# Performance work log

Hardware: AMD Instinct MI355X
Metric: run time of the kernel (lower is better)

The kernel has to match this reference:

```python
import jax, jax.numpy as jnp
import numpy as np

B, S, H = 32, 1024, 512  # batch, src_len, hidden_dim


def setup_inputs() -> dict:
    key = jax.random.key(0)
    k1, k2, k3, k4, k5 = jax.random.split(key, 5)
    hidden = jax.random.normal(k1, (B, H), dtype=jnp.float32)
    encoder_outputs = jax.random.normal(k2, (B, S, 2 * H), dtype=jnp.float32)
    # nn.Linear(3H, H): weight stored here as [3H, H] (input-major) with bias [H]
    W = jax.random.normal(k3, (3 * H, H), dtype=jnp.float32) / np.sqrt(3 * H)
    b = jax.random.normal(k4, (H,), dtype=jnp.float32) * 0.01
    v = jax.random.normal(k5, (H,), dtype=jnp.float32) / np.sqrt(H)
    return {"hidden": hidden, "encoder_outputs": encoder_outputs, "W": W, "b": b, "v": v}


def reference(hidden, encoder_outputs, W, b, v):
    # concat((repeat(hidden), encoder_outputs)) @ W  ==  hidden @ W[:H] (broadcast) + enc @ W[H:]
    Wh, We = W[:H], W[H:]                         # [H,H], [2H,H]
    h_proj = hidden @ Wh                           # [B,H]
    e_proj = jnp.einsum('bse,eh->bsh', encoder_outputs, We)  # [B,S,H]
    energy = jnp.tanh(h_proj[:, None, :] + e_proj + b)       # [B,S,H]
    # bmm(v[B,1,H], energy^T[B,H,S]) -> scores [B,S]
    scores = jnp.einsum('bsh,h->bs', energy, v)
    return jax.nn.softmax(scores, axis=1)
```

## Files before the change

kernel.cpp:

```cpp
#include <hip/hip_runtime.h>
#include <math.h>

#define B_ 32
#define S_ 1024
#define H_ 512
#define K_ 1024
#define M_ (B_ * S_)

typedef __attribute__((ext_vector_type(8))) short bf16x8;
typedef __attribute__((ext_vector_type(4))) float f32x4;

#define AST 40

__device__ __forceinline__ void split_bf16(float f, unsigned short& hi, unsigned short& lo) {
    unsigned u = __float_as_uint(f);
    unsigned rh = (u + 0x7fffu + ((u >> 16) & 1u)) >> 16;
    hi = (unsigned short)rh;
    float fh = __uint_as_float(rh << 16);
    float r = f - fh;
    unsigned ur = __float_as_uint(r);
    unsigned rl = (ur + 0x7fffu + ((ur >> 16) & 1u)) >> 16;
    lo = (unsigned short)rl;
}

__global__ __launch_bounds__(256) void hproj_kernel(
    const float* __restrict__ hidden, const float* __restrict__ W,
    const float* __restrict__ bias, float* __restrict__ hb)
{
    const int tid = threadIdx.x;
    const int h0  = blockIdx.x * 64;
    const int b   = blockIdx.y;
    const int h   = h0 + (tid & 63);
    const int ks  = tid >> 6;
    const float* hrow = hidden + b * H_;
    float acc = 0.f;
    #pragma unroll 8
    for (int k = ks * 128; k < ks * 128 + 128; ++k)
        acc = fmaf(hrow[k], W[(size_t)k * H_ + h], acc);
    __shared__ float red[4][64];
    red[ks][tid & 63] = acc;
    __syncthreads();
    if (tid < 64)
        hb[b * H_ + h0 + tid] = red[0][tid] + red[1][tid] + red[2][tid] + red[3][tid]
                              + bias[h0 + tid];
}

__global__ __launch_bounds__(256) void conv_we_kernel(
    const float* __restrict__ We, unsigned short* __restrict__ Wh,
    unsigned short* __restrict__ Wl)
{
    __shared__ float t[32][33];
    const int tx = threadIdx.x & 31, ty = threadIdx.x >> 5;
    const int k0 = blockIdx.x * 32, n0 = blockIdx.y * 32;
    #pragma unroll
    for (int j = 0; j < 4; ++j) {
        const int k = ty + 8 * j;
        t[k][tx] = We[(size_t)(k0 + k) * H_ + n0 + tx];
    }
    __syncthreads();
    #pragma unroll
    for (int j = 0; j < 4; ++j) {
        const int n = ty + 8 * j;
        unsigned short hi, lo;
        split_bf16(t[tx][n], hi, lo);
        Wh[(size_t)(n0 + n) * K_ + k0 + tx] = hi;
        Wl[(size_t)(n0 + n) * K_ + k0 + tx] = lo;
    }
}

__global__ __launch_bounds__(256, 3) void fused_attn_gemm_mfma(
    const float* __restrict__ EO,
    const unsigned short* __restrict__ Bth,
    const unsigned short* __restrict__ Btl,
    const float* __restrict__ hb,
    const float* __restrict__ v,
    float* __restrict__ partial)
{
    __shared__ unsigned short Ah[128 * AST];
    __shared__ unsigned short Al[128 * AST];
    __shared__ unsigned short Bh[128 * AST];
    __shared__ unsigned short Bl[128 * AST];

    const int tid  = threadIdx.x;
    const int nt   = blockIdx.x;
    const int mt   = blockIdx.y;
    const int row0 = mt * 128;
    const int col0 = nt * 128;
    const int batch = row0 >> 10;

    const int lane   = tid & 63;
    const int wave   = tid >> 6;
    const int wm     = wave >> 1, wn = wave & 1;
    const int lanelo = lane & 15, quad = lane >> 4;

    f32x4 acc[4][4];
    #pragma unroll
    for (int i = 0; i < 4; ++i)
        #pragma unroll
        for (int j = 0; j < 4; ++j)
            acc[i][j] = (f32x4){0.f, 0.f, 0.f, 0.f};

    for (int k0 = 0; k0 < K_; k0 += 32) {
        #pragma unroll
        for (int q = 0; q < 4; ++q) {
            const int f = tid + 256 * q;
            const int m = f >> 3, c = f & 7;
            const float4 av = *reinterpret_cast<const float4*>(
                EO + (size_t)(row0 + m) * K_ + k0 + c * 4);
            union { unsigned short us[4]; uint2 u2; } ph, pl;
            split_bf16(av.x, ph.us[0], pl.us[0]);
            split_bf16(av.y, ph.us[1], pl.us[1]);
            split_bf16(av.z, ph.us[2], pl.us[2]);
            split_bf16(av.w, ph.us[3], pl.us[3]);
            *reinterpret_cast<uint2*>(&Ah[m * AST + c * 4]) = ph.u2;
            *reinterpret_cast<uint2*>(&Al[m * AST + c * 4]) = pl.u2;
        }
        #pragma unroll
        for (int q = 0; q < 2; ++q) {
            const int s = tid + 256 * q;
            const int n = s >> 2, qq = s & 3;
            const size_t g = (size_t)(col0 + n) * K_ + k0 + qq * 8;
            *reinterpret_cast<uint4*>(&Bh[n * AST + qq * 8]) =
                *reinterpret_cast<const uint4*>(Bth + g);
            *reinterpret_cast<uint4*>(&Bl[n * AST + qq * 8]) =
                *reinterpret_cast<const uint4*>(Btl + g);
        }
        __syncthreads();

        bf16x8 a_h[4], a_l[4], b_h[4], b_l[4];
        #pragma unroll
        for (int fi = 0; fi < 4; ++fi) {
            const int m = wm * 64 + fi * 16 + lanelo;
            a_h[fi] = *reinterpret_cast<const bf16x8*>(&Ah[m * AST + quad * 8]);
            a_l[fi] = *reinterpret_cast<const bf16x8*>(&Al[m * AST + quad * 8]);
            const int n = wn * 64 + fi * 16 + lanelo;
            b_h[fi] = *reinterpret_cast<const bf16x8*>(&Bh[n * AST + quad * 8]);
            b_l[fi] = *reinterpret_cast<const bf16x8*>(&Bl[n * AST + quad * 8]);
        }
        #pragma unroll
        for (int fi = 0; fi < 4; ++fi)
            #pragma unroll
            for (int fj = 0; fj < 4; ++fj) {
                acc[fi][fj] = __builtin_amdgcn_mfma_f32_16x16x32_bf16(
                    a_h[fi], b_h[fj], acc[fi][fj], 0, 0, 0);
                acc[fi][fj] = __builtin_amdgcn_mfma_f32_16x16x32_bf16(
                    a_h[fi], b_l[fj], acc[fi][fj], 0, 0, 0);
                acc[fi][fj] = __builtin_amdgcn_mfma_f32_16x16x32_bf16(
                    a_l[fi], b_h[fj], acc[fi][fj], 0, 0, 0);
            }
        __syncthreads();
    }

    const float* hb_row = hb + batch * H_;
    float hbv[4], vv[4];
    #pragma unroll
    for (int fj = 0; fj < 4; ++fj) {
        const int c = col0 + wn * 64 + fj * 16 + lanelo;
        hbv[fj] = hb_row[c];
        vv[fj]  = v[c];
    }
    float* red = reinterpret_cast<float*>(Ah);
    #pragma unroll
    for (int fi = 0; fi < 4; ++fi)
        #pragma unroll
        for (int r = 0; r < 4; ++r) {
            float rs = 0.f;
            #pragma unroll
            for (int fj = 0; fj < 4; ++fj)
                rs = fmaf(tanhf(acc[fi][fj][r] + hbv[fj]), vv[fj], rs);
            rs += __shfl_xor(rs, 1, 64);
            rs += __shfl_xor(rs, 2, 64);
            rs += __shfl_xor(rs, 4, 64);
            rs += __shfl_xor(rs, 8, 64);
            if (lanelo == 0) {
                const int row = wm * 64 + fi * 16 + quad * 4 + r;
                red[row * 2 + wn] = rs;
            }
        }
    __syncthreads();
    if (tid < 128)
        partial[(size_t)nt * M_ + row0 + tid] = red[tid * 2] + red[tid * 2 + 1];
}

#define BM 128
#define BN 128
#define BK 32
#define PAD 4
__global__ __launch_bounds__(256) void fused_attn_gemm_fp32(
    const float* __restrict__ EO, const float* __restrict__ We,
    const float* __restrict__ hb, const float* __restrict__ v,
    float* __restrict__ partial)
{
    __shared__ float As[BK][BM + PAD];
    __shared__ float Bs[BK][BN + PAD];
    const int tid = threadIdx.x;
    const int mt = blockIdx.x, nt = blockIdx.y;
    const int row0 = mt * BM, col0 = nt * BN;
    const int batch = row0 / S_;
    const int tx = tid & 15, ty = tid >> 4;
    float acc[8][8];
    #pragma unroll
    for (int i = 0; i < 8; ++i)
        #pragma unroll
        for (int j = 0; j < 8; ++j) acc[i][j] = 0.0f;
    for (int k0 = 0; k0 < K_; k0 += BK) {
        #pragma unroll
        for (int q = 0; q < 4; ++q) {
            const int f = tid + 256 * q;
            const int m = f >> 3, kq = f & 7;
            const float4 av = *reinterpret_cast<const float4*>(
                EO + (size_t)(row0 + m) * K_ + k0 + kq * 4);
            As[kq * 4 + 0][m] = av.x; As[kq * 4 + 1][m] = av.y;
            As[kq * 4 + 2][m] = av.z; As[kq * 4 + 3][m] = av.w;
        }
        #pragma unroll
        for (int q = 0; q < 4; ++q) {
            const int f = tid + 256 * q;
            const int k = f >> 5, cq = f & 31;
            *reinterpret_cast<float4*>(&Bs[k][cq * 4]) =
                *reinterpret_cast<const float4*>(We + (size_t)(k0 + k) * H_ + col0 + cq * 4);
        }
        __syncthreads();
        #pragma unroll
        for (int kk = 0; kk < BK; ++kk) {
            const float4 a0 = *reinterpret_cast<const float4*>(&As[kk][ty * 4]);
            const float4 a1 = *reinterpret_cast<const float4*>(&As[kk][64 + ty * 4]);
            const float4 b0 = *reinterpret_cast<const float4*>(&Bs[kk][tx * 4]);
            const float4 b1 = *reinterpret_cast<const float4*>(&Bs[kk][64 + tx * 4]);
            const float a[8] = {a0.x, a0.y, a0.z, a0.w, a1.x, a1.y, a1.z, a1.w};
            const float b[8] = {b0.x, b0.y, b0.z, b0.w, b1.x, b1.y, b1.z, b1.w};
            #pragma unroll
            for (int i = 0; i < 8; ++i)
                #pragma unroll
                for (int j = 0; j < 8; ++j)
                    acc[i][j] = fmaf(a[i], b[j], acc[i][j]);
        }
        __syncthreads();
    }
    const float* hb_row = hb + batch * H_;
    float* red = &As[0][0];
    #pragma unroll
    for (int i = 0; i < 8; ++i) {
        const int rloc = (i < 4) ? (ty * 4 + i) : (64 + ty * 4 + i - 4);
        float rs = 0.0f;
        #pragma unroll
        for (int j = 0; j < 8; ++j) {
            const int cloc = (j < 4) ? (tx * 4 + j) : (64 + tx * 4 + j - 4);
            const int c = col0 + cloc;
            rs = fmaf(tanhf(acc[i][j] + hb_row[c]), v[c], rs);
        }
        red[rloc * 17 + tx] = rs;
    }
    __syncthreads();
    if (tid < BM) {
        float s = 0.0f;
        #pragma unroll
        for (int t = 0; t < 16; ++t) s += red[tid * 17 + t];
        partial[(size_t)nt * M_ + row0 + tid] = s;
    }
}

__global__ __launch_bounds__(256) void softmax_kernel(
    const float* __restrict__ partial, float* __restrict__ out)
{
    const int b = blockIdx.x;
    const int tid = threadIdx.x;
    float val[4];
    float lmax = -3.0e38f;
    #pragma unroll
    for (int q = 0; q < 4; ++q) {
        const int idx = b * S_ + tid + 256 * q;
        float sum = partial[idx] + partial[M_ + idx] + partial[2 * M_ + idx] +
                    partial[3 * M_ + idx];
        val[q] = sum;
        lmax = fmaxf(lmax, sum);
    }
    #pragma unroll
    for (int off = 32; off > 0; off >>= 1)
        lmax = fmaxf(lmax, __shfl_down(lmax, off, 64));
    __shared__ float wmax[4];
    if ((tid & 63) == 0) wmax[tid >> 6] = lmax;
    __syncthreads();
    const float gmax = fmaxf(fmaxf(wmax[0], wmax[1]), fmaxf(wmax[2], wmax[3]));
    float lsum = 0.0f;
    #pragma unroll
    for (int q = 0; q < 4; ++q) {
        val[q] = expf(val[q] - gmax);
        lsum += val[q];
    }
    #pragma unroll
    for (int off = 32; off > 0; off >>= 1)
        lsum += __shfl_down(lsum, off, 64);
    __shared__ float wsum[4];
    if ((tid & 63) == 0) wsum[tid >> 6] = lsum;
    __syncthreads();
    const float inv = 1.0f / (wsum[0] + wsum[1] + wsum[2] + wsum[3]);
    #pragma unroll
    for (int q = 0; q < 4; ++q)
        out[b * S_ + tid + 256 * q] = val[q] * inv;
}

extern "C" void kernel_launch(void* const* d_in, const int* in_sizes, int n_in,
                              void* d_out, int out_size, void* d_ws, size_t ws_size,
                              hipStream_t stream) {
    const float* hidden = (const float*)d_in[0];
    const float* EO     = (const float*)d_in[1];
    const float* W      = (const float*)d_in[2];
    const float* bias   = (const float*)d_in[3];
    const float* v      = (const float*)d_in[4];
    float* out          = (float*)d_out;

    float* hb      = (float*)d_ws;
    float* partial = hb + B_ * H_;
    unsigned short* Wth = (unsigned short*)(partial + 4 * M_);
    unsigned short* Wtl = Wth + (size_t)H_ * K_;
    const size_t needed = (size_t)(B_ * H_ + 4 * M_) * sizeof(float)
                        + (size_t)H_ * K_ * 2 * sizeof(unsigned short);

    const float* We = W + (size_t)H_ * H_;

    hproj_kernel<<<dim3(8, B_), 256, 0, stream>>>(hidden, W, bias, hb);
    if (ws_size >= needed) {
        conv_we_kernel<<<dim3(K_ / 32, H_ / 32), 256, 0, stream>>>(We, Wth, Wtl);
        fused_attn_gemm_mfma<<<dim3(4, M_ / 128), 256, 0, stream>>>(EO, Wth, Wtl, hb, v, partial);
    } else {
        fused_attn_gemm_fp32<<<dim3(M_ / BM, 4), 256, 0, stream>>>(EO, We, hb, v, partial);
    }
    softmax_kernel<<<B_, 256, 0, stream>>>(partial, out);
}
```

Before: 327.6 us.

## Pre-split encoder outputs to bf16 hi/lo and stream tiles via async global-to-LDS loads

A separate kernel now converts the encoder outputs once into bf16 hi/lo arrays in workspace. The GEMM then loads A and B tiles straight into LDS with global_load_lds, using an XOR-swizzled layout to avoid bank conflicts. The aim is to drop the per-tile fp32-to-bf16 split (repeated across the 4 column tiles) and the register round trip from the GEMM loop. The cost is an extra pass that reads 128MB and writes 128MB, plus a much larger workspace requirement; the old in-kernel path remains as a fallback and the fp32 fallback is removed.

```diff
diff --git a/kernel.cpp b/kernel.cpp
--- a/kernel.cpp
+++ b/kernel.cpp
@@ -9,8 +9,6 @@
 
 typedef __attribute__((ext_vector_type(8))) short bf16x8;
 typedef __attribute__((ext_vector_type(4))) float f32x4;
-
-#define AST 40
 
 __device__ __forceinline__ void split_bf16(float f, unsigned short& hi, unsigned short& lo) {
     unsigned u = __float_as_uint(f);
@@ -21,6 +19,32 @@
     unsigned ur = __float_as_uint(r);
     unsigned rl = (ur + 0x7fffu + ((ur >> 16) & 1u)) >> 16;
     lo = (unsigned short)rl;
+}
+
+__device__ __forceinline__ void async_copy16(const void* g, void* l) {
+    __builtin_amdgcn_global_load_lds(
+        (const __attribute__((address_space(1))) void*)g,
+        (__attribute__((address_space(3))) void*)l, 16, 0, 0);
+}
+
+__global__ __launch_bounds__(256) void split_eo_kernel(
+    const float* __restrict__ EO, unsigned short* __restrict__ EOh,
+    unsigned short* __restrict__ EOl)
+{
+    const size_t i = ((size_t)blockIdx.x * 256 + threadIdx.x) * 8;
+    const float4 a = *reinterpret_cast<const float4*>(EO + i);
+    const float4 b = *reinterpret_cast<const float4*>(EO + i + 4);
+    union { unsigned short us[8]; uint4 u4; } h, l;
+    split_bf16(a.x, h.us[0], l.us[0]);
+    split_bf16(a.y, h.us[1], l.us[1]);
+    split_bf16(a.z, h.us[2], l.us[2]);
+    split_bf16(a.w, h.us[3], l.us[3]);
+    split_bf16(b.x, h.us[4], l.us[4]);
+    split_bf16(b.y, h.us[5], l.us[5]);
+    split_bf16(b.z, h.us[6], l.us[6]);
+    split_bf16(b.w, h.us[7], l.us[7]);
+    *reinterpret_cast<uint4*>(EOh + i) = h.u4;
+    *reinterpret_cast<uint4*>(EOl + i) = l.u4;
 }
 
 __global__ __launch_bounds__(256) void hproj_kernel(
@@ -68,18 +92,17 @@
     }
 }
 
-__global__ __launch_bounds__(256, 3) void fused_attn_gemm_mfma(
-    const float* __restrict__ EO,
-    const unsigned short* __restrict__ Bth,
-    const unsigned short* __restrict__ Btl,
-    const float* __restrict__ hb,
-    const float* __restrict__ v,
+__global__ __launch_bounds__(256, 3) void gemm_mfma_pre(
+    const unsigned short* __restrict__ EOh, const unsigned short* __restrict__ EOl,
+    const unsigned short* __restrict__ Bth, const unsigned short* __restrict__ Btl,
+    const float* __restrict__ hb, const float* __restrict__ v,
     float* __restrict__ partial)
 {
-    __shared__ unsigned short Ah[128 * AST];
-    __shared__ unsigned short Al[128 * AST];
-    __shared__ unsigned short Bh[128 * AST];
-    __shared__ unsigned short Bl[128 * AST];
+    __shared__ unsigned short lds[4 * 128 * 32];
+    unsigned short* Ah = lds;
+    unsigned short* Al = lds + 4096;
+    unsigned short* Bh = lds + 8192;
+    unsigned short* Bl = lds + 12288;
 
     const int tid  = threadIdx.x;
     const int nt   = blockIdx.x;
@@ -93,6 +116,21 @@
     const int wm     = wave >> 1, wn = wave & 1;
     const int lanelo = lane & 15, quad = lane >> 4;
 
+    const int rl = lane >> 2;
+    const int qs = lane & 3;
+
+    size_t ga[2], gb[2];
+    int ldsoff[2];
+    #pragma unroll
+    for (int j = 0; j < 2; ++j) {
+        const int iss = wave * 2 + j;
+        const int r   = iss * 16 + rl;
+        const int qg  = qs ^ ((r >> 1) & 3);
+        ga[j] = (size_t)(row0 + r) * K_ + qg * 8;
+        gb[j] = (size_t)(col0 + r) * K_ + qg * 8;
+        ldsoff[j] = iss * 512;
+    }
+
     f32x4 acc[4][4];
     #pragma unroll
     for (int i = 0; i < 4; ++i)
@@ -102,40 +140,25 @@
 
     for (int k0 = 0; k0 < K_; k0 += 32) {
         #pragma unroll
-        for (int q = 0; q < 4; ++q) {
-            const int f = tid + 256 * q;
-            const int m = f >> 3, c = f & 7;
-            const float4 av = *reinterpret_cast<const float4*>(
-                EO + (size_t)(row0 + m) * K_ + k0 + c * 4);
-            union { unsigned short us[4]; uint2 u2; } ph, pl;
-            split_bf16(av.x, ph.us[0], pl.us[0]);
-            split_bf16(av.y, ph.us[1], pl.us[1]);
-            split_bf16(av.z, ph.us[2], pl.us[2]);
-            split_bf16(av.w, ph.us[3], pl.us[3]);
-            *reinterpret_cast<uint2*>(&Ah[m * AST + c * 4]) = ph.u2;
-            *reinterpret_cast<uint2*>(&Al[m * AST + c * 4]) = pl.u2;
-        }
-        #pragma unroll
-        for (int q = 0; q < 2; ++q) {
-            const int s = tid + 256 * q;
-            const int n = s >> 2, qq = s & 3;
-            const size_t g = (size_t)(col0 + n) * K_ + k0 + qq * 8;
-            *reinterpret_cast<uint4*>(&Bh[n * AST + qq * 8]) =
-                *reinterpret_cast<const uint4*>(Bth + g);
-            *reinterpret_cast<uint4*>(&Bl[n * AST + qq * 8]) =
-                *reinterpret_cast<const uint4*>(Btl + g);
+        for (int j = 0; j < 2; ++j) {
+            async_copy16(EOh + ga[j] + k0, Ah + ldsoff[j]);
+            async_copy16(EOl + ga[j] + k0, Al + ldsoff[j]);
+            async_copy16(Bth + gb[j] + k0, Bh + ldsoff[j]);
+            async_copy16(Btl + gb[j] + k0, Bl + ldsoff[j]);
         }
         __syncthreads();
 
         bf16x8 a_h[4], a_l[4], b_h[4], b_l[4];
         #pragma unroll
         for (int fi = 0; fi < 4; ++fi) {
-            const int m = wm * 64 + fi * 16 + lanelo;
-            a_h[fi] = *reinterpret_cast<const bf16x8*>(&Ah[m * AST + quad * 8]);
-            a_l[fi] = *reinterpret_cast<const bf16x8*>(&Al[m * AST + quad * 8]);
-            const int n = wn * 64 + fi * 16 + lanelo;
-            b_h[fi] = *reinterpret_cast<const bf16x8*>(&Bh[n * AST + quad * 8]);
-            b_l[fi] = *reinterpret_cast<const bf16x8*>(&Bl[n * AST + quad * 8]);
+            const int m  = wm * 64 + fi * 16 + lanelo;
+            const int sa = quad ^ ((m >> 1) & 3);
+            a_h[fi] = *reinterpret_cast<const bf16x8*>(&Ah[m * 32 + sa * 8]);
+            a_l[fi] = *reinterpret_cast<const bf16x8*>(&Al[m * 32 + sa * 8]);
+            const int n  = wn * 64 + fi * 16 + lanelo;
+            const int sb = quad ^ ((n >> 1) & 3);
+            b_h[fi] = *reinterpret_cast<const bf16x8*>(&Bh[n * 32 + sb * 8]);
+            b_l[fi] = *reinterpret_cast<const bf16x8*>(&Bl[n * 32 + sb * 8]);
         }
         #pragma unroll
         for (int fi = 0; fi < 4; ++fi)
@@ -159,7 +182,7 @@
         hbv[fj] = hb_row[c];
         vv[fj]  = v[c];
     }
-    float* red = reinterpret_cast<float*>(Ah);
+    float* red = reinterpret_cast<float*>(lds);
     #pragma unroll
     for (int fi = 0; fi < 4; ++fi)
         #pragma unroll
@@ -182,82 +205,107 @@
         partial[(size_t)nt * M_ + row0 + tid] = red[tid * 2] + red[tid * 2 + 1];
 }
 
-#define BM 128
-#define BN 128
-#define BK 32
-#define PAD 4
-__global__ __launch_bounds__(256) void fused_attn_gemm_fp32(
-    const float* __restrict__ EO, const float* __restrict__ We,
-    const float* __restrict__ hb, const float* __restrict__ v,
-    float* __restrict__ partial)
-{
-    __shared__ float As[BK][BM + PAD];
-    __shared__ float Bs[BK][BN + PAD];
-    const int tid = threadIdx.x;
-    const int mt = blockIdx.x, nt = blockIdx.y;
-    const int row0 = mt * BM, col0 = nt * BN;
-    const int batch = row0 / S_;
-    const int tx = tid & 15, ty = tid >> 4;
-    float acc[8][8];
-    #pragma unroll
-    for (int i = 0; i < 8; ++i)
-        #pragma unroll
-        for (int j = 0; j < 8; ++j) acc[i][j] = 0.0f;
-    for (int k0 = 0; k0 < K_; k0 += BK) {
+#define AST 40
+__global__ __launch_bounds__(256, 3) void fused_attn_gemm_mfma(
+    const float* __restrict__ EO, const unsigned short* __restrict__ Bth,
+    const unsigned short* __restrict__ Btl, const float* __restrict__ hb,
+    const float* __restrict__ v, float* __restrict__ partial)
+{
+    __shared__ unsigned short Ah[128 * AST];
+    __shared__ unsigned short Al[128 * AST];
+    __shared__ unsigned short Bh[128 * AST];
+    __shared__ unsigned short Bl[128 * AST];
+    const int tid  = threadIdx.x;
+    const int nt   = blockIdx.x;
+    const int mt   = blockIdx.y;
+    const int row0 = mt * 128, col0 = nt * 128;
+    const int batch = row0 >> 10;
+    const int lane = tid & 63, wave = tid >> 6;
+    const int wm = wave >> 1, wn = wave & 1;
+    const int lanelo = lane & 15, quad = lane >> 4;
+    f32x4 acc[4][4];
+    #pragma unroll
+    for (int i = 0; i < 4; ++i)
+        #pragma unroll
+        for (int j = 0; j < 4; ++j) acc[i][j] = (f32x4){0.f, 0.f, 0.f, 0.f};
+    for (int k0 = 0; k0 < K_; k0 += 32) {
         #pragma unroll
         for (int q = 0; q < 4; ++q) {
             const int f = tid + 256 * q;
-            const int m = f >> 3, kq = f & 7;
+            const int m = f >> 3, c = f & 7;
             const float4 av = *reinterpret_cast<const float4*>(
-                EO + (size_t)(row0 + m) * K_ + k0 + kq * 4);
-            As[kq * 4 + 0][m] = av.x; As[kq * 4 + 1][m] = av.y;
-            As[kq * 4 + 2][m] = av.z; As[kq * 4 + 3][m] = av.w;
-        }
-        #pragma unroll
-        for (int q = 0; q < 4; ++q) {
-            const int f = tid + 256 * q;
-            const int k = f >> 5, cq = f & 31;
-            *reinterpret_cast<float4*>(&Bs[k][cq * 4]) =
-                *reinterpret_cast<const float4*>(We + (size_t)(k0 + k) * H_ + col0 + cq * 4);
+                EO + (size_t)(row0 + m) * K_ + k0 + c * 4);
+            union { unsigned short us[4]; uint2 u2; } ph, pl;
+            split_bf16(av.x, ph.us[0], pl.us[0]);
+            split_bf16(av.y, ph.us[1], pl.us[1]);
+            split_bf16(av.z, ph.us[2], pl.us[2]);
+            split_bf16(av.w, ph.us[3], pl.us[3]);
+            *reinterpret_cast<uint2*>(&Ah[m * AST + c * 4]) = ph.u2;
+            *reinterpret_cast<uint2*>(&Al[m * AST + c * 4]) = pl.u2;
+        }
+        #pragma unroll
+        for (int q = 0; q < 2; ++q) {
+            const int s = tid + 256 * q;
+            const int n = s >> 2, qq = s & 3;
+            const size_t g = (size_t)(col0 + n) * K_ + k0 + qq * 8;
+            *reinterpret_cast<uint4*>(&Bh[n * AST + qq * 8]) =
+                *reinterpret_cast<const uint4*>(Bth + g);
+            *reinterpret_cast<uint4*>(&Bl[n * AST + qq * 8]) =
+                *reinterpret_cast<const uint4*>(Btl + g);
         }
         __syncthreads();
-        #pragma unroll
-        for (int kk = 0; kk < BK; ++kk) {
-            const float4 a0 = *reinterpret_cast<const float4*>(&As[kk][ty * 4]);
-            const float4 a1 = *reinterpret_cast<const float4*>(&As[kk][64 + ty * 4]);
-            const float4 b0 = *reinterpret_cast<const float4*>(&Bs[kk][tx * 4]);
-            const float4 b1 = *reinterpret_cast<const float4*>(&Bs[kk][64 + tx * 4]);
-            const float a[8] = {a0.x, a0.y, a0.z, a0.w, a1.x, a1.y, a1.z, a1.w};
-            const float b[8] = {b0.x, b0.y, b0.z, b0.w, b1.x, b1.y, b1.z, b1.w};
+        bf16x8 a_h[4], a_l[4], b_h[4], b_l[4];
+        #pragma unroll
+        for (int fi = 0; fi < 4; ++fi) {
+            const int m = wm * 64 + fi * 16 + lanelo;
+            a_h[fi] = *reinterpret_cast<const bf16x8*>(&Ah[m * AST + quad * 8]);
+            a_l[fi] = *reinterpret_cast<const bf16x8*>(&Al[m * AST + quad * 8]);
+            const int n = wn * 64 + fi * 16 + lanelo;
+            b_h[fi] = *reinterpret_cast<const bf16x8*>(&Bh[n * AST + quad * 8]);
+            b_l[fi] = *reinterpret_cast<const bf16x8*>(&Bl[n * AST + quad * 8]);
+        }
+        #pragma unroll
+        for (int fi = 0; fi < 4; ++fi)
             #pragma unroll
-            for (int i = 0; i < 8; ++i)
-                #pragma unroll
-                for (int j = 0; j < 8; ++j)
-                    acc[i][j] = fmaf(a[i], b[j], acc[i][j]);
-        }
+            for (int fj = 0; fj < 4; ++fj) {
+                acc[fi][fj] = __builtin_amdgcn_mfma_f32_16x16x32_bf16(
+                    a_h[fi], b_h[fj], acc[fi][fj], 0, 0, 0);
+                acc[fi][fj] = __builtin_amdgcn_mfma_f32_16x16x32_bf16(
+                    a_h[fi], b_l[fj], acc[fi][fj], 0, 0, 0);
+                acc[fi][fj] = __builtin_amdgcn_mfma_f32_16x16x32_bf16(
+                    a_l[fi], b_h[fj], acc[fi][fj], 0, 0, 0);
+            }
         __syncthreads();
     }
     const float* hb_row = hb + batch * H_;
-    float* red = &As[0][0];
-    #pragma unroll
-    for (int i = 0; i < 8; ++i) {
-        const int rloc = (i < 4) ? (ty * 4 + i) : (64 + ty * 4 + i - 4);
-        float rs = 0.0f;
-        #pragma unroll
-        for (int j = 0; j < 8; ++j) {
-            const int cloc = (j < 4) ? (tx * 4 + j) : (64 + tx * 4 + j - 4);
-            const int c = col0 + cloc;
-            rs = fmaf(tanhf(acc[i][j] + hb_row[c]), v[c], rs);
-        }
-        red[rloc * 17 + tx] = rs;
-    }
-    __syncthreads();
-    if (tid < BM) {
-        float s = 0.0f;
-        #pragma unroll
-        for (int t = 0; t < 16; ++t) s += red[tid * 17 + t];
-        partial[(size_t)nt * M_ + row0 + tid] = s;
-    }
+    float hbv[4], vv[4];
+    #pragma unroll
+    for (int fj = 0; fj < 4; ++fj) {
+        const int c = col0 + wn * 64 + fj * 16 + lanelo;
+        hbv[fj] = hb_row[c];
+        vv[fj]  = v[c];
+    }
+    float* red = reinterpret_cast<float*>(Ah);
+    #pragma unroll
+    for (int fi = 0; fi < 4; ++fi)
+        #pragma unroll
+        for (int r = 0; r < 4; ++r) {
+            float rs = 0.f;
+            #pragma unroll
+            for (int fj = 0; fj < 4; ++fj)
+                rs = fmaf(tanhf(acc[fi][fj][r] + hbv[fj]), vv[fj], rs);
+            rs += __shfl_xor(rs, 1, 64);
+            rs += __shfl_xor(rs, 2, 64);
+            rs += __shfl_xor(rs, 4, 64);
+            rs += __shfl_xor(rs, 8, 64);
+            if (lanelo == 0) {
+                const int row = wm * 64 + fi * 16 + quad * 4 + r;
+                red[row * 2 + wn] = rs;
+            }
+        }
+    __syncthreads();
+    if (tid < 128)
+        partial[(size_t)nt * M_ + row0 + tid] = red[tid * 2] + red[tid * 2 + 1];
 }
 
 __global__ __launch_bounds__(256) void softmax_kernel(
@@ -314,17 +362,23 @@
     float* partial = hb + B_ * H_;
     unsigned short* Wth = (unsigned short*)(partial + 4 * M_);
     unsigned short* Wtl = Wth + (size_t)H_ * K_;
-    const size_t needed = (size_t)(B_ * H_ + 4 * M_) * sizeof(float)
-                        + (size_t)H_ * K_ * 2 * sizeof(unsigned short);
+    unsigned short* EOh = Wtl + (size_t)H_ * K_;
+    unsigned short* EOl = EOh + (size_t)M_ * K_;
+
+    const size_t need_small = (size_t)(B_ * H_ + 4 * M_) * sizeof(float)
+                            + (size_t)H_ * K_ * 2 * sizeof(unsigned short);
+    const size_t need_full  = need_small
+                            + (size_t)M_ * K_ * 2 * sizeof(unsigned short);
 
     const float* We = W + (size_t)H_ * H_;
 
     hproj_kernel<<<dim3(8, B_), 256, 0, stream>>>(hidden, W, bias, hb);
-    if (ws_size >= needed) {
-        conv_we_kernel<<<dim3(K_ / 32, H_ / 32), 256, 0, stream>>>(We, Wth, Wtl);
+    conv_we_kernel<<<dim3(K_ / 32, H_ / 32), 256, 0, stream>>>(We, Wth, Wtl);
+    if (ws_size >= need_full) {
+        split_eo_kernel<<<(size_t)M_ * K_ / (256 * 8), 256, 0, stream>>>(EO, EOh, EOl);
+        gemm_mfma_pre<<<dim3(4, M_ / 128), 256, 0, stream>>>(EOh, EOl, Wth, Wtl, hb, v, partial);
+    } else {
         fused_attn_gemm_mfma<<<dim3(4, M_ / 128), 256, 0, stream>>>(EO, Wth, Wtl, hb, v, partial);
-    } else {
-        fused_attn_gemm_fp32<<<dim3(M_ / BM, 4), 256, 0, stream>>>(EO, We, hb, v, partial);
     }
     softmax_kernel<<<B_, 256, 0, stream>>>(partial, out);
 }
```

After: 354.6 us. 1.08x slower.

## Double-buffer MFMA GEMM with async B loads, swizzled LDS, merged prep kernels

Applied to the files above, without the earlier changes.

Restructures the main split-bf16 MFMA GEMM into a double-buffered pipeline. The next EO tile is loaded into registers and the next weight tiles are copied straight to LDS with global_load_lds while the current tile is computed, which removes one barrier per k-step. LDS padding is replaced by an XOR swizzle, and occupancy is lowered to 2 blocks per SM because LDS use doubles. The hidden-projection and weight-conversion kernels are merged into one launch, and the fp32 fallback path and its workspace size check are removed.

```diff
diff --git a/kernel.cpp b/kernel.cpp
--- a/kernel.cpp
+++ b/kernel.cpp
@@ -9,8 +9,6 @@
 
 typedef __attribute__((ext_vector_type(8))) short bf16x8;
 typedef __attribute__((ext_vector_type(4))) float f32x4;
-
-#define AST 40
 
 __device__ __forceinline__ void split_bf16(float f, unsigned short& hi, unsigned short& lo) {
     unsigned u = __float_as_uint(f);
@@ -23,63 +21,82 @@
     lo = (unsigned short)rl;
 }
 
-__global__ __launch_bounds__(256) void hproj_kernel(
+__device__ __forceinline__ void split8_store(const float4& x, const float4& y,
+                                             unsigned short* hiP, unsigned short* loP) {
+    union { unsigned short us[8]; uint4 u; } h, l;
+    split_bf16(x.x, h.us[0], l.us[0]);
+    split_bf16(x.y, h.us[1], l.us[1]);
+    split_bf16(x.z, h.us[2], l.us[2]);
+    split_bf16(x.w, h.us[3], l.us[3]);
+    split_bf16(y.x, h.us[4], l.us[4]);
+    split_bf16(y.y, h.us[5], l.us[5]);
+    split_bf16(y.z, h.us[6], l.us[6]);
+    split_bf16(y.w, h.us[7], l.us[7]);
+    *reinterpret_cast<uint4*>(hiP) = h.u;
+    *reinterpret_cast<uint4*>(loP) = l.u;
+}
+
+__device__ __forceinline__ void async_copy16(const void* g, void* l) {
+    __builtin_amdgcn_global_load_lds(
+        (const __attribute__((address_space(1))) void*)g,
+        (__attribute__((address_space(3))) void*)l, 16, 0, 0);
+}
+
+__global__ __launch_bounds__(256) void prep_kernel(
     const float* __restrict__ hidden, const float* __restrict__ W,
-    const float* __restrict__ bias, float* __restrict__ hb)
+    const float* __restrict__ bias, float* __restrict__ hb,
+    unsigned short* __restrict__ Wh, unsigned short* __restrict__ Wl)
 {
-    const int tid = threadIdx.x;
-    const int h0  = blockIdx.x * 64;
-    const int b   = blockIdx.y;
-    const int h   = h0 + (tid & 63);
-    const int ks  = tid >> 6;
-    const float* hrow = hidden + b * H_;
-    float acc = 0.f;
-    #pragma unroll 8
-    for (int k = ks * 128; k < ks * 128 + 128; ++k)
-        acc = fmaf(hrow[k], W[(size_t)k * H_ + h], acc);
     __shared__ float red[4][64];
-    red[ks][tid & 63] = acc;
-    __syncthreads();
-    if (tid < 64)
-        hb[b * H_ + h0 + tid] = red[0][tid] + red[1][tid] + red[2][tid] + red[3][tid]
-                              + bias[h0 + tid];
-}
-
-__global__ __launch_bounds__(256) void conv_we_kernel(
-    const float* __restrict__ We, unsigned short* __restrict__ Wh,
-    unsigned short* __restrict__ Wl)
-{
     __shared__ float t[32][33];
-    const int tx = threadIdx.x & 31, ty = threadIdx.x >> 5;
-    const int k0 = blockIdx.x * 32, n0 = blockIdx.y * 32;
-    #pragma unroll
-    for (int j = 0; j < 4; ++j) {
-        const int k = ty + 8 * j;
-        t[k][tx] = We[(size_t)(k0 + k) * H_ + n0 + tx];
-    }
-    __syncthreads();
-    #pragma unroll
-    for (int j = 0; j < 4; ++j) {
-        const int n = ty + 8 * j;
-        unsigned short hi, lo;
-        split_bf16(t[tx][n], hi, lo);
-        Wh[(size_t)(n0 + n) * K_ + k0 + tx] = hi;
-        Wl[(size_t)(n0 + n) * K_ + k0 + tx] = lo;
-    }
-}
-
-__global__ __launch_bounds__(256, 3) void fused_attn_gemm_mfma(
+    const int bx = blockIdx.x;
+    if (bx < 256) {
+        const int tid = threadIdx.x;
+        const int h0  = (bx & 7) * 64;
+        const int b   = bx >> 3;
+        const int h   = h0 + (tid & 63);
+        const int ks  = tid >> 6;
+        const float* hrow = hidden + b * H_;
+        float acc = 0.f;
+        #pragma unroll 8
+        for (int k = ks * 128; k < ks * 128 + 128; ++k)
+            acc = fmaf(hrow[k], W[(size_t)k * H_ + h], acc);
+        red[ks][tid & 63] = acc;
+        __syncthreads();
+        if (tid < 64)
+            hb[b * H_ + h0 + tid] = red[0][tid] + red[1][tid] + red[2][tid]
+                                  + red[3][tid] + bias[h0 + tid];
+    } else {
+        const float* We = W + (size_t)H_ * H_;
+        const int cx = bx - 256;
+        const int k0 = (cx & 31) * 32, n0 = (cx >> 5) * 32;
+        const int tx = threadIdx.x & 31, ty = threadIdx.x >> 5;
+        #pragma unroll
+        for (int j = 0; j < 4; ++j) {
+            const int k = ty + 8 * j;
+            t[k][tx] = We[(size_t)(k0 + k) * H_ + n0 + tx];
+        }
+        __syncthreads();
+        #pragma unroll
+        for (int j = 0; j < 4; ++j) {
+            const int n = ty + 8 * j;
+            unsigned short hi, lo;
+            split_bf16(t[tx][n], hi, lo);
+            Wh[(size_t)(n0 + n) * K_ + k0 + tx] = hi;
+            Wl[(size_t)(n0 + n) * K_ + k0 + tx] = lo;
+        }
+    }
+}
+
+__global__ __launch_bounds__(256, 2) void gemm_fused(
     const float* __restrict__ EO,
     const unsigned short* __restrict__ Bth,
     const unsigned short* __restrict__ Btl,
-    const float* __restrict__ hb,
-    const float* __restrict__ v,
+    const float* __restrict__ hb, const float* __restrict__ v,
     float* __restrict__ partial)
 {
-    __shared__ unsigned short Ah[128 * AST];
-    __shared__ unsigned short Al[128 * AST];
-    __shared__ unsigned short Bh[128 * AST];
-    __shared__ unsigned short Bl[128 * AST];
+    __shared__ unsigned short ldsA[2][2][4096];
+    __shared__ unsigned short ldsB[2][2][4096];
 
     const int tid  = threadIdx.x;
     const int nt   = blockIdx.x;
@@ -93,6 +110,26 @@
     const int wm     = wave >> 1, wn = wave & 1;
     const int lanelo = lane & 15, quad = lane >> 4;
 
+    size_t gaA[2];
+    int offA[2];
+    #pragma unroll
+    for (int s = 0; s < 2; ++s) {
+        const int seg = tid + 256 * s;
+        const int m = seg >> 2, sg = seg & 3;
+        gaA[s] = (size_t)(row0 + m) * K_ + sg * 8;
+        offA[s] = m * 32 + (sg ^ ((m >> 1) & 3)) * 8;
+    }
+    size_t gb[2];
+    int offB[2];
+    #pragma unroll
+    for (int j = 0; j < 2; ++j) {
+        const int iss = wave * 2 + j;
+        const int r   = iss * 16 + (lane >> 2);
+        const int qg  = (lane & 3) ^ ((r >> 1) & 3);
+        gb[j] = (size_t)(col0 + r) * K_ + qg * 8;
+        offB[j] = iss * 512;
+    }
+
     f32x4 acc[4][4];
     #pragma unroll
     for (int i = 0; i < 4; ++i)
@@ -100,42 +137,49 @@
         for (int j = 0; j < 4; ++j)
             acc[i][j] = (f32x4){0.f, 0.f, 0.f, 0.f};
 
-    for (int k0 = 0; k0 < K_; k0 += 32) {
-        #pragma unroll
-        for (int q = 0; q < 4; ++q) {
-            const int f = tid + 256 * q;
-            const int m = f >> 3, c = f & 7;
-            const float4 av = *reinterpret_cast<const float4*>(
-                EO + (size_t)(row0 + m) * K_ + k0 + c * 4);
-            union { unsigned short us[4]; uint2 u2; } ph, pl;
-            split_bf16(av.x, ph.us[0], pl.us[0]);
-            split_bf16(av.y, ph.us[1], pl.us[1]);
-            split_bf16(av.z, ph.us[2], pl.us[2]);
-            split_bf16(av.w, ph.us[3], pl.us[3]);
-            *reinterpret_cast<uint2*>(&Ah[m * AST + c * 4]) = ph.u2;
-            *reinterpret_cast<uint2*>(&Al[m * AST + c * 4]) = pl.u2;
-        }
-        #pragma unroll
-        for (int q = 0; q < 2; ++q) {
-            const int s = tid + 256 * q;
-            const int n = s >> 2, qq = s & 3;
-            const size_t g = (size_t)(col0 + n) * K_ + k0 + qq * 8;
-            *reinterpret_cast<uint4*>(&Bh[n * AST + qq * 8]) =
-                *reinterpret_cast<const uint4*>(Bth + g);
-            *reinterpret_cast<uint4*>(&Bl[n * AST + qq * 8]) =
-                *reinterpret_cast<const uint4*>(Btl + g);
-        }
+    float4 a0[2], a1[2];
+    #pragma unroll
+    for (int s = 0; s < 2; ++s) {
+        a0[s] = *reinterpret_cast<const float4*>(EO + gaA[s]);
+        a1[s] = *reinterpret_cast<const float4*>(EO + gaA[s] + 4);
+    }
+    #pragma unroll
+    for (int j = 0; j < 2; ++j) {
+        async_copy16(Bth + gb[j], &ldsB[0][0][offB[j]]);
+        async_copy16(Btl + gb[j], &ldsB[0][1][offB[j]]);
+    }
+    #pragma unroll
+    for (int s = 0; s < 2; ++s)
+        split8_store(a0[s], a1[s], &ldsA[0][0][offA[s]], &ldsA[0][1][offA[s]]);
+
+    for (int i = 0; i < 32; ++i) {
         __syncthreads();
+        const int cur = i & 1, nxt = cur ^ 1;
+        const int k0n = 32 * (i + 1);
+        if (i < 31) {
+            #pragma unroll
+            for (int s = 0; s < 2; ++s) {
+                a0[s] = *reinterpret_cast<const float4*>(EO + gaA[s] + k0n);
+                a1[s] = *reinterpret_cast<const float4*>(EO + gaA[s] + k0n + 4);
+            }
+            #pragma unroll
+            for (int j = 0; j < 2; ++j) {
+                async_copy16(Bth + gb[j] + k0n, &ldsB[nxt][0][offB[j]]);
+                async_copy16(Btl + gb[j] + k0n, &ldsB[nxt][1][offB[j]]);
+            }
+        }
 
         bf16x8 a_h[4], a_l[4], b_h[4], b_l[4];
         #pragma unroll
         for (int fi = 0; fi < 4; ++fi) {
-            const int m = wm * 64 + fi * 16 + lanelo;
-            a_h[fi] = *reinterpret_cast<const bf16x8*>(&Ah[m * AST + quad * 8]);
-            a_l[fi] = *reinterpret_cast<const bf16x8*>(&Al[m * AST + quad * 8]);
-            const int n = wn * 64 + fi * 16 + lanelo;
-            b_h[fi] = *reinterpret_cast<const bf16x8*>(&Bh[n * AST + quad * 8]);
-            b_l[fi] = *reinterpret_cast<const bf16x8*>(&Bl[n * AST + quad * 8]);
+            const int m  = wm * 64 + fi * 16 + lanelo;
+            const int sa = quad ^ ((m >> 1) & 3);
+            a_h[fi] = *reinterpret_cast<const bf16x8*>(&ldsA[cur][0][m * 32 + sa * 8]);
+            a_l[fi] = *reinterpret_cast<const bf16x8*>(&ldsA[cur][1][m * 32 + sa * 8]);
+            const int n  = wn * 64 + fi * 16 + lanelo;
+            const int sb = quad ^ ((n >> 1) & 3);
+            b_h[fi] = *reinterpret_cast<const bf16x8*>(&ldsB[cur][0][n * 32 + sb * 8]);
+            b_l[fi] = *reinterpret_cast<const bf16x8*>(&ldsB[cur][1][n * 32 + sb * 8]);
         }
         #pragma unroll
         for (int fi = 0; fi < 4; ++fi)
@@ -148,7 +192,13 @@
                 acc[fi][fj] = __builtin_amdgcn_mfma_f32_16x16x32_bf16(
                     a_l[fi], b_h[fj], acc[fi][fj], 0, 0, 0);
             }
-        __syncthreads();
+
+        if (i < 31) {
+            #pragma unroll
+            for (int s = 0; s < 2; ++s)
+                split8_store(a0[s], a1[s],
+                             &ldsA[nxt][0][offA[s]], &ldsA[nxt][1][offA[s]]);
+        }
     }
 
     const float* hb_row = hb + batch * H_;
@@ -159,7 +209,7 @@
         hbv[fj] = hb_row[c];
         vv[fj]  = v[c];
     }
-    float* red = reinterpret_cast<float*>(Ah);
+    float* red = reinterpret_cast<float*>(&ldsA[0][0][0]);
     #pragma unroll
     for (int fi = 0; fi < 4; ++fi)
         #pragma unroll
@@ -182,84 +232,6 @@
         partial[(size_t)nt * M_ + row0 + tid] = red[tid * 2] + red[tid * 2 + 1];
 }
 
-#define BM 128
-#define BN 128
-#define BK 32
-#define PAD 4
-__global__ __launch_bounds__(256) void fused_attn_gemm_fp32(
-    const float* __restrict__ EO, const float* __restrict__ We,
-    const float* __restrict__ hb, const float* __restrict__ v,
-    float* __restrict__ partial)
-{
-    __shared__ float As[BK][BM + PAD];
-    __shared__ float Bs[BK][BN + PAD];
-    const int tid = threadIdx.x;
-    const int mt = blockIdx.x, nt = blockIdx.y;
-    const int row0 = mt * BM, col0 = nt * BN;
-    const int batch = row0 / S_;
-    const int tx = tid & 15, ty = tid >> 4;
-    float acc[8][8];
-    #pragma unroll
-    for (int i = 0; i < 8; ++i)
-        #pragma unroll
-        for (int j = 0; j < 8; ++j) acc[i][j] = 0.0f;
-    for (int k0 = 0; k0 < K_; k0 += BK) {
-        #pragma unroll
-        for (int q = 0; q < 4; ++q) {
-            const int f = tid + 256 * q;
-            const int m = f >> 3, kq = f & 7;
-            const float4 av = *reinterpret_cast<const float4*>(
-                EO + (size_t)(row0 + m) * K_ + k0 + kq * 4);
-            As[kq * 4 + 0][m] = av.x; As[kq * 4 + 1][m] = av.y;
-            As[kq * 4 + 2][m] = av.z; As[kq * 4 + 3][m] = av.w;
-        }
-        #pragma unroll
-        for (int q = 0; q < 4; ++q) {
-            const int f = tid + 256 * q;
-            const int k = f >> 5, cq = f & 31;
-            *reinterpret_cast<float4*>(&Bs[k][cq * 4]) =
-                *reinterpret_cast<const float4*>(We + (size_t)(k0 + k) * H_ + col0 + cq * 4);
-        }
-        __syncthreads();
-        #pragma unroll
-        for (int kk = 0; kk < BK; ++kk) {
-            const float4 a0 = *reinterpret_cast<const float4*>(&As[kk][ty * 4]);
-            const float4 a1 = *reinterpret_cast<const float4*>(&As[kk][64 + ty * 4]);
-            const float4 b0 = *reinterpret_cast<const float4*>(&Bs[kk][tx * 4]);
-            const float4 b1 = *reinterpret_cast<const float4*>(&Bs[kk][64 + tx * 4]);
-            const float a[8] = {a0.x, a0.y, a0.z, a0.w, a1.x, a1.y, a1.z, a1.w};
-            const float b[8] = {b0.x, b0.y, b0.z, b0.w, b1.x, b1.y, b1.z, b1.w};
-            #pragma unroll
-            for (int i = 0; i < 8; ++i)
-                #pragma unroll
-                for (int j = 0; j < 8; ++j)
-                    acc[i][j] = fmaf(a[i], b[j], acc[i][j]);
-        }
-        __syncthreads();
-    }
-    const float* hb_row = hb + batch * H_;
-    float* red = &As[0][0];
-    #pragma unroll
-    for (int i = 0; i < 8; ++i) {
-        const int rloc = (i < 4) ? (ty * 4 + i) : (64 + ty * 4 + i - 4);
-        float rs = 0.0f;
-        #pragma unroll
-        for (int j = 0; j < 8; ++j) {
-            const int cloc = (j < 4) ? (tx * 4 + j) : (64 + tx * 4 + j - 4);
-            const int c = col0 + cloc;
-            rs = fmaf(tanhf(acc[i][j] + hb_row[c]), v[c], rs);
-        }
-        red[rloc * 17 + tx] = rs;
-    }
-    __syncthreads();
-    if (tid < BM) {
-        float s = 0.0f;
-        #pragma unroll
-        for (int t = 0; t < 16; ++t) s += red[tid * 17 + t];
-        partial[(size_t)nt * M_ + row0 + tid] = s;
-    }
-}
-
 __global__ __launch_bounds__(256) void softmax_kernel(
     const float* __restrict__ partial, float* __restrict__ out)
 {
@@ -314,17 +286,8 @@
     float* partial = hb + B_ * H_;
     unsigned short* Wth = (unsigned short*)(partial + 4 * M_);
     unsigned short* Wtl = Wth + (size_t)H_ * K_;
-    const size_t needed = (size_t)(B_ * H_ + 4 * M_) * sizeof(float)
-                        + (size_t)H_ * K_ * 2 * sizeof(unsigned short);
-
-    const float* We = W + (size_t)H_ * H_;
-
-    hproj_kernel<<<dim3(8, B_), 256, 0, stream>>>(hidden, W, bias, hb);
-    if (ws_size >= needed) {
-        conv_we_kernel<<<dim3(K_ / 32, H_ / 32), 256, 0, stream>>>(We, Wth, Wtl);
-        fused_attn_gemm_mfma<<<dim3(4, M_ / 128), 256, 0, stream>>>(EO, Wth, Wtl, hb, v, partial);
-    } else {
-        fused_attn_gemm_fp32<<<dim3(M_ / BM, 4), 256, 0, stream>>>(EO, We, hb, v, partial);
-    }
+
+    prep_kernel<<<768, 256, 0, stream>>>(hidden, W, bias, hb, Wth, Wtl);
+    gemm_fused<<<dim3(4, M_ / 128), 256, 0, stream>>>(EO, Wth, Wtl, hb, v, partial);
     softmax_kernel<<<B_, 256, 0, stream>>>(partial, out);
 }
```

Measured after the change: 317.0 us. 1.03x faster.
